# Optimization experiments

Measured on AMD Instinct MI355X. Metric: run time of the kernel, lower is better.

Reference implementation:

```python
import jax, jax.numpy as jnp
import numpy as np

B, C, H, G = 4, 128, 8, 64
F = G * G  # 4096 faces on a GxG grid mesh surrogate
DH = C // H


def _build_rings():
    # BFS rings on a GxG 4-neighbor grid from face 0 (corner): ring r = {(i,j): i+j == r}
    rings_list = []
    for r in range(2 * G - 1):
        lo, hi = max(0, r - G + 1), min(r, G - 1)
        rings_list.append([i * G + (r - i) for i in range(lo, hi + 1)])
    n_rings = len(rings_list)
    max_ring = max(len(rr) for rr in rings_list)
    rings = np.full((n_rings, max_ring), -1, dtype=np.int64)
    sizes = np.zeros((n_rings,), dtype=np.int64)
    for r, rr in enumerate(rings_list):
        rings[r, :len(rr)] = rr
        sizes[r] = len(rr)
    return rings, sizes


def setup_inputs() -> dict:
    key = jax.random.key(0)
    ks = jax.random.split(key, 6)
    s = 1.0 / np.sqrt(C)
    x = jax.random.normal(ks[0], (B, C, F), dtype=jnp.float32)
    Wq0 = jax.random.normal(ks[1], (C, C), dtype=jnp.float32) * s
    Wk0 = jax.random.normal(ks[2], (C, C), dtype=jnp.float32) * s
    Wv0 = jax.random.normal(ks[3], (C, C), dtype=jnp.float32) * s
    Wq1 = jax.random.normal(ks[4], (C, C), dtype=jnp.float32) * s
    Wk1 = jax.random.normal(ks[5], (C, C), dtype=jnp.float32) * s
    rings, sizes = _build_rings()
    return {"x": x, "Wq0": Wq0, "Wk0": Wk0, "Wv0": Wv0, "Wq1": Wq1, "Wk1": Wk1,
            "rings": jnp.asarray(rings), "ring_sizes": jnp.asarray(sizes)}


def _attend(q_in, kv_in, Wq, Wk, Wv):
    # AnchorAttentionBlock, mode='resid': MHA(q=q_in, kv=kv_in) + q_in
    Bq, Cc, Nq = q_in.shape
    Nk = kv_in.shape[2]
    q = jnp.einsum('oc,bcn->bon', Wq, q_in).reshape(Bq, H, DH, Nq)
    k = jnp.einsum('oc,bcn->bon', Wk, kv_in).reshape(Bq, H, DH, Nk)
    v = jnp.einsum('oc,bcn->bon', Wv, kv_in).reshape(Bq, H, DH, Nk)
    a = jax.nn.softmax(jnp.einsum('bhdq,bhdk->bhqk', q, k) / np.float32(np.sqrt(DH)), axis=-1)
    o = jnp.einsum('bhqk,bhdk->bhdq', a, v).reshape(Bq, Cc, Nq)
    return o + q_in


def _cos_map(q_in, kv_in, Wq, Wk):
    # return_map=True, normalize=True -> per-head cosine similarity map in [-1, 1]
    Bq, _, Nq = q_in.shape
    Nk = kv_in.shape[2]
    q = jnp.einsum('oc,bcn->bon', Wq, q_in).reshape(Bq, H, DH, Nq)
    k = jnp.einsum('oc,bcn->bon', Wk, kv_in).reshape(Bq, H, DH, Nk)
    qn = q * jax.lax.rsqrt(jnp.sum(q * q, axis=2, keepdims=True) + 1e-8)
    kn = k * jax.lax.rsqrt(jnp.sum(k * k, axis=2, keepdims=True) + 1e-8)
    return jnp.einsum('bhdq,bhdk->bhqk', qn, kn)  # [B,H,Nq,Nk]


def reference(x, Wq0, Wk0, Wv0, Wq1, Wk1, rings, ring_sizes):
    rings_np = np.asarray(rings)
    sizes_np = np.asarray(ring_sizes)
    feats = x
    # Sequential BFS flood-fill: per ring, boundary faces attend over all faces.
    # Vectorized over the batch (all meshes share the grid topology + anchor).
    for r in range(rings_np.shape[0]):
        ring = rings_np[r, :int(sizes_np[r])]          # concrete face indices of this ring
        bf = feats[:, :, ring]                          # [B, C, Nb] boundary features
        bf = _attend(bf, feats, Wq0, Wk0, Wv0)          # kv = all faces (current state)
        feats = feats.at[:, :, ring].set(bf)
    anchor = int(rings_np[0, 0])
    anchor_x = feats[:, :, anchor:anchor + 1]           # [B, C, 1]
    q_x = _attend(x, anchor_x, Wq0, Wk0, Wv0)           # attention[:-1] pass on raw x
    m = _cos_map(q_x, anchor_x, Wq1, Wk1)               # [B, H, F, 1] in [-1, 1]
    final_scores = jnp.mean((m + 1.0) * 0.5, axis=1)    # [B, F, 1] in [0, 1]
    return feats, final_scores
```

## Files before the change

### kernel.cpp

```cpp
#include <hip/hip_runtime.h>
#include <hip/hip_bf16.h>

#define Bn 4
#define Cn 128
#define Fn 4096
#define NRINGS 127

typedef short bhalf4 __attribute__((ext_vector_type(4)));
typedef float f32x4  __attribute__((ext_vector_type(4)));

#define OFF_K   1048576
#define OFF_V   2097152
#define OFF_PM  3145728
#define OFF_PL  3211264
#define OFF_PO  3276800
#define OFF_VA  4325376
#define OFF_KN  4325888

__device__ __forceinline__ ushort f2bf(float f) {
    __hip_bfloat16 h = __float2bfloat16(f);
    return *reinterpret_cast<ushort*>(&h);
}

__global__ __launch_bounds__(512, 2) void initQKV(
    const float* __restrict__ x, const float* __restrict__ Wq0,
    const float* __restrict__ Wk0, const float* __restrict__ Wv0,
    ushort* __restrict__ Q0bf, ushort* __restrict__ Kbf, ushort* __restrict__ Vbf)
{
    __shared__ float xs[Cn * 64];
    const int wg = blockIdx.x, t = threadIdx.x;
    const int b = wg >> 6, n0 = (wg & 63) << 6;
    for (int idx = t; idx < Cn * 64; idx += 512) {
        int c = idx >> 6, j = idx & 63;
        xs[idx] = x[(((b << 7) + c) << 12) + n0 + j];
    }
    __syncthreads();
    const int o = t & 127, j0 = (t >> 7) << 4;
    float aq[16], ak[16], av[16];
#pragma unroll
    for (int k = 0; k < 16; ++k) { aq[k] = 0.f; ak[k] = 0.f; av[k] = 0.f; }
    for (int c = 0; c < Cn; ++c) {
        float wq = Wq0[(o << 7) + c];
        float wk = Wk0[(o << 7) + c];
        float wv = Wv0[(o << 7) + c];
        const float* xr = &xs[(c << 6) + j0];
#pragma unroll
        for (int k = 0; k < 16; ++k) {
            float xv = xr[k];
            aq[k] += wq * xv; ak[k] += wk * xv; av[k] += wv * xv;
        }
    }
    const int h = o >> 4, d = o & 15;
    const int bh = (b << 3) + h;
#pragma unroll
    for (int k = 0; k < 16; ++k) {
        int col = n0 + j0 + k;
        int qi = ((bh << 12) + col) * 16 + d;
        Q0bf[qi] = f2bf(aq[k]);
        Kbf[qi]  = f2bf(ak[k]);
    }
    uint vv[8];
#pragma unroll
    for (int k2 = 0; k2 < 8; ++k2)
        vv[k2] = (uint)f2bf(av[2*k2]) | ((uint)f2bf(av[2*k2+1]) << 16);
    uint4* dst = (uint4*)&Vbf[(((bh << 4) + d) << 12) + n0 + j0];
    dst[0] = make_uint4(vv[0], vv[1], vv[2], vv[3]);
    dst[1] = make_uint4(vv[4], vv[5], vv[6], vv[7]);
}

template<bool TAIL>
__global__ __launch_bounds__(512, 2) void fusedRing(
    const float* __restrict__ x, const float* __restrict__ Wk0,
    const float* __restrict__ Wv0, const int* __restrict__ rings,
    const int* __restrict__ rsz, const ushort* __restrict__ Q0bf,
    ushort* __restrict__ Kbf, ushort* __restrict__ Vbf,
    float* __restrict__ pm, float* __restrict__ pl, float* __restrict__ po,
    float* __restrict__ feats, int r)
{
    __shared__ ushort Kls[512 * 24];
    __shared__ ushort Vls[16 * 520];
    __shared__ ushort Qls[64 * 24];
    __shared__ float  outc[4 * 128];
    __shared__ int colsC[64], colsF[64];
    __shared__ int ownIdx[64];
    __shared__ int ownCnt;

    const int t = threadIdx.x, wgid = blockIdx.x;
    const int b = wgid >> 6, h = (wgid >> 3) & 7, sp = wgid & 7;
    const int bh = (b << 3) + h;
    const int n  = TAIL ? 0 : rsz[r];
    const int np = (r > 0) ? rsz[r - 1] : 0;
    const int keybase = sp << 9;

    if (t < 64) colsC[t] = (r > 0 && t < np) ? rings[(r-1)*64 + t] : -1;
    else if (t < 128) { int q = t - 64; colsF[q] = (!TAIL && q < n) ? rings[r*64 + q] : -1; }
    if (t == 0) ownCnt = 0;
    __syncthreads();

    if (!TAIL) {
        {
            const uint4* src = (const uint4*)(Kbf + ((bh << 12) + keybase + t) * 16);
            uint4 a0 = src[0], a1 = src[1];
            *(uint4*)&Kls[t*24]     = a0;
            *(uint4*)&Kls[t*24 + 8] = a1;
        }
        {
            int d = t >> 5, c32 = t & 31;
            const uint4* src = (const uint4*)(Vbf + (((bh << 4) + d) << 12) + keybase + (c32 << 4));
            uint4 a0 = src[0], a1 = src[1];
            *(uint4*)&Vls[d*520 + (c32 << 4)]     = a0;
            *(uint4*)&Vls[d*520 + (c32 << 4) + 8] = a1;
        }
        if (t < 128) {
            int q = t >> 1, half = t & 1;
            int cq = colsF[q];
            uint4 qv = make_uint4(0u, 0u, 0u, 0u);
            if (cq >= 0)
                qv = *(const uint4*)(Q0bf + ((bh << 12) + cq) * 16 + half * 8);
            *(uint4*)&Qls[q*24 + half*8] = qv;
        }
    }
    __syncthreads();

    if (r > 0) {
        const int bufp = (r - 1) & 1;
        if (t < np) {
            int cq = colsC[t];
            if (cq >= keybase && cq < keybase + 512) {
                int slot = atomicAdd(&ownCnt, 1);
                ownIdx[slot] = t;
            }
        }
        __syncthreads();
        const int cnt = ownCnt;
        for (int base = 0; base < cnt; base += 4) {
            {
                int slot = t >> 7, c = t & 127;
                int ow = base + slot;
                if (ow < cnt) {
                    int j = ownIdx[ow];
                    int col = colsC[j];
                    int hh = c >> 4, dd = c & 15;
                    int p0 = ((bufp << 5) + (b << 3) + hh) * 1024 + j;
                    float mstar = -1e30f;
#pragma unroll
                    for (int s2 = 0; s2 < 16; ++s2)
                        mstar = fmaxf(mstar, pm[p0 + (s2 << 6)]);
                    float lstar = 0.f, osum = 0.f;
#pragma unroll
                    for (int s2 = 0; s2 < 16; ++s2) {
                        int pi = p0 + (s2 << 6);
                        float e = __expf(pm[pi] - mstar);
                        lstar += pl[pi] * e;
                        osum  += po[(pi << 4) + dd] * e;
                    }
                    float outv = osum / lstar + x[(((b << 7) + c) << 12) + col];
                    outc[(slot << 7) + c] = outv;
                    if (h == 0) feats[(((b << 7) + c) << 12) + col] = outv;
                }
            }
            __syncthreads();
            if (!TAIL && t < 128) {
                int slot = t >> 5;
                int ow = base + slot;
                if (ow < cnt) {
                    int task = t & 31;
                    int isV = task >> 4, dd = task & 15;
                    int col = colsC[ownIdx[ow]];
                    const float* W = isV ? Wv0 : Wk0;
                    const float* oc = &outc[slot << 7];
                    int row = (h << 4) + dd;
                    float acc = 0.f;
                    for (int c2 = 0; c2 < Cn; ++c2)
                        acc += W[(row << 7) + c2] * oc[c2];
                    ushort bfv = f2bf(acc);
                    if (isV) {
                        Vbf[(((bh << 4) + dd) << 12) + col] = bfv;
                        Vls[dd*520 + (col - keybase)] = bfv;
                    } else {
                        Kbf[((bh << 12) + col) * 16 + dd] = bfv;
                        Kls[(col - keybase)*24 + dd] = bfv;
                    }
                }
            }
            __syncthreads();
        }
    }
    if (TAIL) return;

    const int w = t >> 6, lane = t & 63;
    const int qt = w & 3, kh = w >> 2;
    const int buf = r & 1;
    if (qt * 16 < n) {
        const int lm = lane & 15, lg = lane >> 4;
        bhalf4 qf = *(const bhalf4*)&Qls[(qt*16 + lm)*24 + (lg << 2)];
        const int key0 = kh << 8;
        f32x4 sc[16];
#pragma unroll
        for (int kt = 0; kt < 16; ++kt) {
            bhalf4 kf = *(const bhalf4*)&Kls[(key0 + (kt << 4) + lm)*24 + (lg << 2)];
            f32x4 z = {0.f, 0.f, 0.f, 0.f};
            sc[kt] = __builtin_amdgcn_mfma_f32_16x16x16bf16_1k(kf, qf, z, 0, 0, 0);
        }
        float m = -1e30f;
#pragma unroll
        for (int kt = 0; kt < 16; ++kt) {
            m = fmaxf(m, fmaxf(fmaxf(sc[kt][0], sc[kt][1]), fmaxf(sc[kt][2], sc[kt][3])));
        }
        m = fmaxf(m, __shfl_xor(m, 16));
        m = fmaxf(m, __shfl_xor(m, 32));
        float lsum = 0.f;
        bhalf4 pf[16];
#pragma unroll
        for (int kt = 0; kt < 16; ++kt) {
            float p0 = __expf((sc[kt][0] - m) * 0.25f);
            float p1 = __expf((sc[kt][1] - m) * 0.25f);
            float p2 = __expf((sc[kt][2] - m) * 0.25f);
            float p3 = __expf((sc[kt][3] - m) * 0.25f);
            lsum += (p0 + p1) + (p2 + p3);
            bhalf4 pv;
            pv[0] = (short)f2bf(p0); pv[1] = (short)f2bf(p1);
            pv[2] = (short)f2bf(p2); pv[3] = (short)f2bf(p3);
            pf[kt] = pv;
        }
        lsum += __shfl_xor(lsum, 16);
        lsum += __shfl_xor(lsum, 32);
        f32x4 oacc = {0.f, 0.f, 0.f, 0.f};
#pragma unroll
        for (int kt = 0; kt < 16; ++kt) {
            bhalf4 vf = *(const bhalf4*)&Vls[lm*520 + key0 + (kt << 4) + (lg << 2)];
            oacc = __builtin_amdgcn_mfma_f32_16x16x16bf16_1k(pf[kt], vf, oacc, 0, 0, 0);
        }
        const int pb = ((((buf << 5) + bh) << 4) | ((sp << 1) + kh)) * 64;
        if (lg == 0) {
            pm[pb + qt*16 + lm] = m * 0.25f;
            pl[pb + qt*16 + lm] = lsum;
        }
#pragma unroll
        for (int reg = 0; reg < 4; ++reg)
            po[(pb + qt*16 + (lg << 2) + reg) * 16 + lm] = oacc[reg];
    }
}

__global__ __launch_bounds__(128) void epi1(
    const float* __restrict__ feats, const float* __restrict__ Wv0,
    const float* __restrict__ Wk1, const int* __restrict__ rings,
    float* __restrict__ Va, float* __restrict__ Kn)
{
    int b = blockIdx.x;
    int i = threadIdx.x;
    int anchor = rings[0];
    __shared__ float la[128];
    __shared__ float kk2[128];
    la[i] = feats[((b * Cn + i) << 12) + anchor];
    __syncthreads();
    float va = 0.f, k1 = 0.f;
    for (int c = 0; c < 128; ++c) {
        va += Wv0[i * 128 + c] * la[c];
        k1 += Wk1[i * 128 + c] * la[c];
    }
    Va[b * 128 + i] = va;
    kk2[i] = k1 * k1;
    __syncthreads();
    float ss = 0.f;
    int hb = i & ~15;
    for (int d = 0; d < 16; ++d) ss += kk2[hb + d];
    Kn[b * 128 + i] = k1 * rsqrtf(ss + 1e-8f);
}

__global__ __launch_bounds__(256) void epi2(
    const float* __restrict__ x, const float* __restrict__ Wq1,
    const float* __restrict__ Va, const float* __restrict__ Kn,
    float* __restrict__ scores)
{
    __shared__ float Wt[128 * 132];
    __shared__ float lxT[128 * 36];
    const int bid = blockIdx.x, t = threadIdx.x;
    const int b = bid >> 7, col0 = (bid & 127) << 5;
    for (int idx = t; idx < 128 * 128; idx += 256) {
        int o = idx >> 7, c = idx & 127;
        Wt[c*132 + o] = Wq1[idx];
    }
    for (int idx = t; idx < 128 * 32; idx += 256) {
        int c = idx >> 5, col = idx & 31;
        lxT[c*36 + col] = x[(((b << 7) + c) << 12) + col0 + col] + Va[(b << 7) + c];
    }
    __syncthreads();
    const int og = t & 31, colg = t >> 5;
    const int o0 = og << 2, cl0 = colg << 2;
    float acc[4][4];
#pragma unroll
    for (int i = 0; i < 4; ++i)
#pragma unroll
        for (int j = 0; j < 4; ++j) acc[i][j] = 0.f;
    for (int c = 0; c < 128; ++c) {
        f32x4 wv = *(const f32x4*)&Wt[c*132 + o0];
        f32x4 xv = *(const f32x4*)&lxT[c*36 + cl0];
#pragma unroll
        for (int i = 0; i < 4; ++i)
#pragma unroll
            for (int j = 0; j < 4; ++j) acc[i][j] += wv[i] * xv[j];
    }
    float kn4[4];
#pragma unroll
    for (int i = 0; i < 4; ++i) kn4[i] = Kn[(b << 7) + o0 + i];
    float res[4];
#pragma unroll
    for (int j = 0; j < 4; ++j) {
        float ss = acc[0][j]*acc[0][j] + acc[1][j]*acc[1][j]
                 + acc[2][j]*acc[2][j] + acc[3][j]*acc[3][j];
        ss += __shfl_xor(ss, 1);
        ss += __shfl_xor(ss, 2);
        float rs = rsqrtf(ss + 1e-8f);
        float mp = (acc[0][j]*kn4[0] + acc[1][j]*kn4[1]
                  + acc[2][j]*kn4[2] + acc[3][j]*kn4[3]) * rs;
#pragma unroll
        for (int msk = 1; msk <= 16; msk <<= 1) mp += __shfl_xor(mp, msk);
        res[j] = 0.5f + mp * (1.0f / 16.0f);
    }
    if (og == 0) {
#pragma unroll
        for (int j = 0; j < 4; ++j)
            scores[(b << 12) + col0 + cl0 + j] = res[j];
    }
}

extern "C" void kernel_launch(void* const* d_in, const int* in_sizes, int n_in,
                              void* d_out, int out_size, void* d_ws, size_t ws_size,
                              hipStream_t stream) {
    const float* x   = (const float*)d_in[0];
    const float* Wq0 = (const float*)d_in[1];
    const float* Wk0 = (const float*)d_in[2];
    const float* Wv0 = (const float*)d_in[3];
    const float* Wq1 = (const float*)d_in[4];
    const float* Wk1 = (const float*)d_in[5];
    const int*   rings = (const int*)d_in[6];
    const int*   rsz   = (const int*)d_in[7];

    float* feats  = (float*)d_out;
    float* scores = feats + Bn * Cn * Fn;

    float*  ws   = (float*)d_ws;
    ushort* Q0bf = (ushort*)ws;
    ushort* Kbf  = (ushort*)(ws + OFF_K);
    ushort* Vbf  = (ushort*)(ws + OFF_V);
    float*  pm   = ws + OFF_PM;
    float*  pl   = ws + OFF_PL;
    float*  po   = ws + OFF_PO;
    float*  Va   = ws + OFF_VA;
    float*  Kn   = ws + OFF_KN;

    initQKV<<<256, 512, 0, stream>>>(x, Wq0, Wk0, Wv0, Q0bf, Kbf, Vbf);

    for (int r = 0; r < NRINGS; ++r) {
        fusedRing<false><<<256, 512, 0, stream>>>(
            x, Wk0, Wv0, rings, rsz, Q0bf, Kbf, Vbf, pm, pl, po, feats, r);
    }
    fusedRing<true><<<256, 512, 0, stream>>>(
        x, Wk0, Wv0, rings, rsz, Q0bf, Kbf, Vbf, pm, pl, po, feats, NRINGS);

    epi1<<<Bn, 128, 0, stream>>>(feats, Wv0, Wk1, rings, Va, Kn);
    epi2<<<512, 256, 0, stream>>>(x, Wq1, Va, Kn, scores);
}
```

Baseline: 1.781 ms.

## Read K/V/Q fragments directly from global memory and parallelize ring K/V update

The ring kernel no longer stages the whole 512-key K and V slice and the Q tile into LDS on every launch. The MFMA loops now load fragments straight from global (L2-resident) buffers, and a threadfence plus barrier makes freshly written K/V visible first. The per-face K/V projection update is spread over all 512 threads, each summing a quarter of the channels with shuffle reductions. initQKV also tiles the weight matrices through LDS instead of reading them from global per thread. This trades a per-launch LDS fill and the extra barriers for scattered, less-coalesced global fragment loads.

```diff
diff --git a/kernel.cpp b/kernel.cpp
--- a/kernel.cpp
+++ b/kernel.cpp
@@ -28,28 +28,40 @@
     ushort* __restrict__ Q0bf, ushort* __restrict__ Kbf, ushort* __restrict__ Vbf)
 {
     __shared__ float xs[Cn * 64];
+    __shared__ float Wls[3 * 128 * 33];
     const int wg = blockIdx.x, t = threadIdx.x;
     const int b = wg >> 6, n0 = (wg & 63) << 6;
     for (int idx = t; idx < Cn * 64; idx += 512) {
         int c = idx >> 6, j = idx & 63;
         xs[idx] = x[(((b << 7) + c) << 12) + n0 + j];
     }
-    __syncthreads();
     const int o = t & 127, j0 = (t >> 7) << 4;
     float aq[16], ak[16], av[16];
 #pragma unroll
     for (int k = 0; k < 16; ++k) { aq[k] = 0.f; ak[k] = 0.f; av[k] = 0.f; }
-    for (int c = 0; c < Cn; ++c) {
-        float wq = Wq0[(o << 7) + c];
-        float wk = Wk0[(o << 7) + c];
-        float wv = Wv0[(o << 7) + c];
-        const float* xr = &xs[(c << 6) + j0];
-#pragma unroll
-        for (int k = 0; k < 16; ++k) {
-            float xv = xr[k];
-            aq[k] += wq * xv; ak[k] += wk * xv; av[k] += wv * xv;
-        }
-    }
+
+    for (int cc = 0; cc < 128; cc += 32) {
+        __syncthreads();
+        for (int idx = t; idx < 128 * 32; idx += 512) {
+            int oo = idx >> 5, jj = idx & 31;
+            Wls[oo * 33 + jj]                = Wq0[(oo << 7) + cc + jj];
+            Wls[128 * 33 + oo * 33 + jj]     = Wk0[(oo << 7) + cc + jj];
+            Wls[2 * 128 * 33 + oo * 33 + jj] = Wv0[(oo << 7) + cc + jj];
+        }
+        __syncthreads();
+        for (int c2 = 0; c2 < 32; ++c2) {
+            float wq = Wls[o * 33 + c2];
+            float wk = Wls[128 * 33 + o * 33 + c2];
+            float wv = Wls[2 * 128 * 33 + o * 33 + c2];
+            const float* xr = &xs[((cc + c2) << 6) + j0];
+#pragma unroll
+            for (int k = 0; k < 16; ++k) {
+                float xv = xr[k];
+                aq[k] += wq * xv; ak[k] += wk * xv; av[k] += wv * xv;
+            }
+        }
+    }
+
     const int h = o >> 4, d = o & 15;
     const int bh = (b << 3) + h;
 #pragma unroll
@@ -77,10 +89,7 @@
     float* __restrict__ pm, float* __restrict__ pl, float* __restrict__ po,
     float* __restrict__ feats, int r)
 {
-    __shared__ ushort Kls[512 * 24];
-    __shared__ ushort Vls[16 * 520];
-    __shared__ ushort Qls[64 * 24];
-    __shared__ float  outc[4 * 128];
+    __shared__ float outc[4 * 128];
     __shared__ int colsC[64], colsF[64];
     __shared__ int ownIdx[64];
     __shared__ int ownCnt;
@@ -93,33 +102,8 @@
     const int keybase = sp << 9;
 
     if (t < 64) colsC[t] = (r > 0 && t < np) ? rings[(r-1)*64 + t] : -1;
-    else if (t < 128) { int q = t - 64; colsF[q] = (!TAIL && q < n) ? rings[r*64 + q] : -1; }
+    else if (t < 128) { int q = t - 64; colsF[q] = (!TAIL && q < n) ? rings[r*64 + q] : 0; }
     if (t == 0) ownCnt = 0;
-    __syncthreads();
-
-    if (!TAIL) {
-        {
-            const uint4* src = (const uint4*)(Kbf + ((bh << 12) + keybase + t) * 16);
-            uint4 a0 = src[0], a1 = src[1];
-            *(uint4*)&Kls[t*24]     = a0;
-            *(uint4*)&Kls[t*24 + 8] = a1;
-        }
-        {
-            int d = t >> 5, c32 = t & 31;
-            const uint4* src = (const uint4*)(Vbf + (((bh << 4) + d) << 12) + keybase + (c32 << 4));
-            uint4 a0 = src[0], a1 = src[1];
-            *(uint4*)&Vls[d*520 + (c32 << 4)]     = a0;
-            *(uint4*)&Vls[d*520 + (c32 << 4) + 8] = a1;
-        }
-        if (t < 128) {
-            int q = t >> 1, half = t & 1;
-            int cq = colsF[q];
-            uint4 qv = make_uint4(0u, 0u, 0u, 0u);
-            if (cq >= 0)
-                qv = *(const uint4*)(Q0bf + ((bh << 12) + cq) * 16 + half * 8);
-            *(uint4*)&Qls[q*24 + half*8] = qv;
-        }
-    }
     __syncthreads();
 
     if (r > 0) {
@@ -160,26 +144,27 @@
                 }
             }
             __syncthreads();
-            if (!TAIL && t < 128) {
-                int slot = t >> 5;
+            if (!TAIL) {
+                int slot = t >> 7, rem = t & 127;
+                int task = rem >> 2, quarter = rem & 3;
                 int ow = base + slot;
                 if (ow < cnt) {
-                    int task = t & 31;
                     int isV = task >> 4, dd = task & 15;
                     int col = colsC[ownIdx[ow]];
+                    int row = (h << 4) + dd;
                     const float* W = isV ? Wv0 : Wk0;
                     const float* oc = &outc[slot << 7];
-                    int row = (h << 4) + dd;
                     float acc = 0.f;
-                    for (int c2 = 0; c2 < Cn; ++c2)
-                        acc += W[(row << 7) + c2] * oc[c2];
-                    ushort bfv = f2bf(acc);
-                    if (isV) {
-                        Vbf[(((bh << 4) + dd) << 12) + col] = bfv;
-                        Vls[dd*520 + (col - keybase)] = bfv;
-                    } else {
-                        Kbf[((bh << 12) + col) * 16 + dd] = bfv;
-                        Kls[(col - keybase)*24 + dd] = bfv;
+                    int c0 = quarter << 5;
+#pragma unroll
+                    for (int c2 = 0; c2 < 32; ++c2)
+                        acc += W[(row << 7) + c0 + c2] * oc[c0 + c2];
+                    acc += __shfl_xor(acc, 1);
+                    acc += __shfl_xor(acc, 2);
+                    if (quarter == 0) {
+                        ushort bfv = f2bf(acc);
+                        if (isV) Vbf[(((bh << 4) + dd) << 12) + col] = bfv;
+                        else     Kbf[((bh << 12) + col) * 16 + dd] = bfv;
                     }
                 }
             }
@@ -187,26 +172,30 @@
         }
     }
     if (TAIL) return;
+
+    __threadfence();
+    __syncthreads();
 
     const int w = t >> 6, lane = t & 63;
     const int qt = w & 3, kh = w >> 2;
     const int buf = r & 1;
     if (qt * 16 < n) {
         const int lm = lane & 15, lg = lane >> 4;
-        bhalf4 qf = *(const bhalf4*)&Qls[(qt*16 + lm)*24 + (lg << 2)];
-        const int key0 = kh << 8;
+        const int cq = colsF[qt * 16 + lm];
+        bhalf4 qf = *(const bhalf4*)&Q0bf[(((bh << 12) + cq) << 4) + (lg << 2)];
+        const int key0 = keybase + (kh << 8);
         f32x4 sc[16];
 #pragma unroll
         for (int kt = 0; kt < 16; ++kt) {
-            bhalf4 kf = *(const bhalf4*)&Kls[(key0 + (kt << 4) + lm)*24 + (lg << 2)];
+            bhalf4 kf = *(const bhalf4*)
+                &Kbf[(((bh << 12) + key0 + (kt << 4) + lm) << 4) + (lg << 2)];
             f32x4 z = {0.f, 0.f, 0.f, 0.f};
             sc[kt] = __builtin_amdgcn_mfma_f32_16x16x16bf16_1k(kf, qf, z, 0, 0, 0);
         }
         float m = -1e30f;
 #pragma unroll
-        for (int kt = 0; kt < 16; ++kt) {
+        for (int kt = 0; kt < 16; ++kt)
             m = fmaxf(m, fmaxf(fmaxf(sc[kt][0], sc[kt][1]), fmaxf(sc[kt][2], sc[kt][3])));
-        }
         m = fmaxf(m, __shfl_xor(m, 16));
         m = fmaxf(m, __shfl_xor(m, 32));
         float lsum = 0.f;
@@ -228,7 +217,8 @@
         f32x4 oacc = {0.f, 0.f, 0.f, 0.f};
 #pragma unroll
         for (int kt = 0; kt < 16; ++kt) {
-            bhalf4 vf = *(const bhalf4*)&Vls[lm*520 + key0 + (kt << 4) + (lg << 2)];
+            bhalf4 vf = *(const bhalf4*)
+                &Vbf[(((bh << 4) + lm) << 12) + key0 + (kt << 4) + (lg << 2)];
             oacc = __builtin_amdgcn_mfma_f32_16x16x16bf16_1k(pf[kt], vf, oacc, 0, 0, 0);
         }
         const int pb = ((((buf << 5) + bh) << 4) | ((sp << 1) + kh)) * 64;
```

Result: slower. 5.727 ms (+221.5%).

## Replace per-ring kernel launches with persistent cooperative kernel using grid barriers

Applied to the files above, without the earlier changes.

Runs the 127-ring sequential flood-fill inside one cooperative persistent kernel of 64 workgroups. Each workgroup keeps its 2048-key K/V slice resident in LDS across rings, and rings are separated by software global barriers instead of kernel launches. This is meant to remove per-launch overhead and the repeated reload of K/V tiles each ring. The cost is far fewer workgroups (64 vs 256), so each does more serial flash work, and it adds two spin barriers per ring. initQKV also now stages the weights through LDS in chunks, and the multi-launch path is kept as a fallback if the cooperative launch fails.

```diff
diff --git a/kernel.cpp b/kernel.cpp
--- a/kernel.cpp
+++ b/kernel.cpp
@@ -5,17 +5,20 @@
 #define Cn 128
 #define Fn 4096
 #define NRINGS 127
+#define NWG 64
 
 typedef short bhalf4 __attribute__((ext_vector_type(4)));
 typedef float f32x4  __attribute__((ext_vector_type(4)));
 
-#define OFF_K   1048576
-#define OFF_V   2097152
-#define OFF_PM  3145728
-#define OFF_PL  3211264
-#define OFF_PO  3276800
-#define OFF_VA  4325376
-#define OFF_KN  4325888
+#define OFF_K    1048576
+#define OFF_V    2097152
+#define OFF_PM   3145728
+#define OFF_PL   3211264
+#define OFF_PO   3276800
+#define OFF_OUTC 4325376
+#define OFF_VA   4358144
+#define OFF_KN   4358656
+#define OFF_BAR  4359168
 
 __device__ __forceinline__ ushort f2bf(float f) {
     __hip_bfloat16 h = __float2bfloat16(f);
@@ -25,29 +28,41 @@
 __global__ __launch_bounds__(512, 2) void initQKV(
     const float* __restrict__ x, const float* __restrict__ Wq0,
     const float* __restrict__ Wk0, const float* __restrict__ Wv0,
-    ushort* __restrict__ Q0bf, ushort* __restrict__ Kbf, ushort* __restrict__ Vbf)
+    ushort* __restrict__ Q0bf, ushort* __restrict__ Kbf, ushort* __restrict__ Vbf,
+    int* __restrict__ bar)
 {
     __shared__ float xs[Cn * 64];
+    __shared__ float Wls[3 * 128 * 33];
     const int wg = blockIdx.x, t = threadIdx.x;
+    if (wg == 0 && t == 0) bar[0] = 0;
     const int b = wg >> 6, n0 = (wg & 63) << 6;
     for (int idx = t; idx < Cn * 64; idx += 512) {
         int c = idx >> 6, j = idx & 63;
         xs[idx] = x[(((b << 7) + c) << 12) + n0 + j];
     }
-    __syncthreads();
     const int o = t & 127, j0 = (t >> 7) << 4;
     float aq[16], ak[16], av[16];
 #pragma unroll
     for (int k = 0; k < 16; ++k) { aq[k] = 0.f; ak[k] = 0.f; av[k] = 0.f; }
-    for (int c = 0; c < Cn; ++c) {
-        float wq = Wq0[(o << 7) + c];
-        float wk = Wk0[(o << 7) + c];
-        float wv = Wv0[(o << 7) + c];
-        const float* xr = &xs[(c << 6) + j0];
-#pragma unroll
-        for (int k = 0; k < 16; ++k) {
-            float xv = xr[k];
-            aq[k] += wq * xv; ak[k] += wk * xv; av[k] += wv * xv;
+    for (int cc = 0; cc < 128; cc += 32) {
+        __syncthreads();
+        for (int idx = t; idx < 128 * 32; idx += 512) {
+            int oo = idx >> 5, jj = idx & 31;
+            Wls[oo * 33 + jj]                = Wq0[(oo << 7) + cc + jj];
+            Wls[128 * 33 + oo * 33 + jj]     = Wk0[(oo << 7) + cc + jj];
+            Wls[2 * 128 * 33 + oo * 33 + jj] = Wv0[(oo << 7) + cc + jj];
+        }
+        __syncthreads();
+        for (int c2 = 0; c2 < 32; ++c2) {
+            float wq = Wls[o * 33 + c2];
+            float wk = Wls[128 * 33 + o * 33 + c2];
+            float wv = Wls[2 * 128 * 33 + o * 33 + c2];
+            const float* xr = &xs[((cc + c2) << 6) + j0];
+#pragma unroll
+            for (int k = 0; k < 16; ++k) {
+                float xv = xr[k];
+                aq[k] += wq * xv; ak[k] += wk * xv; av[k] += wv * xv;
+            }
         }
     }
     const int h = o >> 4, d = o & 15;
@@ -68,8 +83,223 @@
     dst[1] = make_uint4(vv[4], vv[5], vv[6], vv[7]);
 }
 
+__device__ __forceinline__ void gbar(int* bar, int target) {
+    __syncthreads();
+    if (threadIdx.x == 0) {
+        __threadfence();
+        __hip_atomic_fetch_add(bar, 1, __ATOMIC_RELEASE, __HIP_MEMORY_SCOPE_AGENT);
+        while (__hip_atomic_load(bar, __ATOMIC_RELAXED, __HIP_MEMORY_SCOPE_AGENT) < target)
+            __builtin_amdgcn_s_sleep(2);
+        __threadfence();
+    }
+    __syncthreads();
+}
+
+__device__ __forceinline__ void flashStep(
+    int n, int buf, int bh, int kv, int t,
+    const ushort* qs, const ushort* Kls, const ushort* Vls,
+    float* __restrict__ pm, float* __restrict__ pl, float* __restrict__ po)
+{
+    const int w = t >> 6, lane = t & 63;
+    const int qt = w & 3, kq = w >> 2;
+    if (qt * 16 >= n) return;
+    const int lm = lane & 15, lg = lane >> 4;
+    bhalf4 qf = *(const bhalf4*)&qs[(qt * 16 + lm) * 20 + (lg << 2)];
+    const int kbase = kq << 10;
+
+    float m = -3e38f;
+#pragma unroll 4
+    for (int kt = 0; kt < 64; ++kt) {
+        bhalf4 kf = *(const bhalf4*)&Kls[(kbase + (kt << 4) + lm) * 20 + (lg << 2)];
+        f32x4 z = {0.f, 0.f, 0.f, 0.f};
+        f32x4 s = __builtin_amdgcn_mfma_f32_16x16x16bf16_1k(kf, qf, z, 0, 0, 0);
+        m = fmaxf(m, fmaxf(fmaxf(s[0], s[1]), fmaxf(s[2], s[3])));
+    }
+    m = fmaxf(m, __shfl_xor(m, 16));
+    m = fmaxf(m, __shfl_xor(m, 32));
+
+    float lsum = 0.f;
+    f32x4 oacc = {0.f, 0.f, 0.f, 0.f};
+#pragma unroll 4
+    for (int kt = 0; kt < 64; ++kt) {
+        bhalf4 kf = *(const bhalf4*)&Kls[(kbase + (kt << 4) + lm) * 20 + (lg << 2)];
+        f32x4 z = {0.f, 0.f, 0.f, 0.f};
+        f32x4 s = __builtin_amdgcn_mfma_f32_16x16x16bf16_1k(kf, qf, z, 0, 0, 0);
+        float p0 = __expf((s[0] - m) * 0.25f);
+        float p1 = __expf((s[1] - m) * 0.25f);
+        float p2 = __expf((s[2] - m) * 0.25f);
+        float p3 = __expf((s[3] - m) * 0.25f);
+        lsum += (p0 + p1) + (p2 + p3);
+        bhalf4 pv;
+        pv[0] = (short)f2bf(p0); pv[1] = (short)f2bf(p1);
+        pv[2] = (short)f2bf(p2); pv[3] = (short)f2bf(p3);
+        bhalf4 vf = *(const bhalf4*)&Vls[lm * 2056 + kbase + (kt << 4) + (lg << 2)];
+        oacc = __builtin_amdgcn_mfma_f32_16x16x16bf16_1k(pv, vf, oacc, 0, 0, 0);
+    }
+    lsum += __shfl_xor(lsum, 16);
+    lsum += __shfl_xor(lsum, 32);
+
+    const int sl = (kv << 1) + kq;
+    const int pb = ((((buf << 5) + bh) << 2) + sl) * 64;
+    if (lg == 0) {
+        pm[pb + qt * 16 + lm] = m * 0.25f;
+        pl[pb + qt * 16 + lm] = lsum;
+    }
+#pragma unroll
+    for (int reg = 0; reg < 4; ++reg)
+        po[(pb + qt * 16 + (lg << 2) + reg) * 16 + lm] = oacc[reg];
+}
+
+__device__ __forceinline__ void combineP1(
+    int np, int bufp, int b, int h, int kv, int t,
+    const int* colsC, const float* __restrict__ x,
+    const float* __restrict__ pm, const float* __restrict__ pl,
+    const float* __restrict__ po, float* __restrict__ outcG,
+    float* __restrict__ feats)
+{
+    int jj = t >> 4, dd = t & 15;
+    int jq = (kv << 5) + jj;
+    if (jq >= np) return;
+    int bh = (b << 3) + h;
+    int col = colsC[jq];
+    int p0 = ((((bufp << 5) + bh) << 2) << 6) + jq;
+    float mstar = -3e38f;
+#pragma unroll
+    for (int sl = 0; sl < 4; ++sl) mstar = fmaxf(mstar, pm[p0 + (sl << 6)]);
+    float lstar = 0.f, osum = 0.f;
+#pragma unroll
+    for (int sl = 0; sl < 4; ++sl) {
+        int pi = p0 + (sl << 6);
+        float e = __expf(pm[pi] - mstar);
+        lstar += pl[pi] * e;
+        osum  += po[(pi << 4) + dd] * e;
+    }
+    float outv = osum / lstar + x[(((b << 7) + (h << 4) + dd) << 12) + col];
+    outcG[(((b << 6) + jq) << 7) + (h << 4) + dd] = outv;
+    feats[(((b << 7) + (h << 4) + dd) << 12) + col] = outv;
+}
+
+__device__ __forceinline__ void patchP2(
+    int np, int b, int h, int kv, int t,
+    const int* colsC, int* ownIdx, int* ownCnt,
+    const float* __restrict__ Wk0, const float* __restrict__ Wv0,
+    const float* __restrict__ outcG, ushort* Kls, ushort* Vls)
+{
+    const int keyG0 = kv << 11;
+    if (t < np) {
+        int cq = colsC[t];
+        if (cq >= keyG0 && cq < keyG0 + 2048)
+            ownIdx[atomicAdd(ownCnt, 1)] = t;
+    }
+    __syncthreads();
+    const int cnt = *ownCnt;
+    const int slot = t >> 6, rr = (t >> 1) & 31, half = t & 1;
+    const int dd = rr & 15;
+    for (int base = 0; base < cnt; base += 8) {
+        int ow = base + slot;
+        if (ow < cnt) {
+            int jq = ownIdx[ow];
+            int col = colsC[jq];
+            const float* W = (rr < 16) ? Wk0 : Wv0;
+            int row = (h << 4) + dd;
+            const f32x4* W4  = (const f32x4*)&W[(row << 7) + (half << 6)];
+            const f32x4* oc4 = (const f32x4*)&outcG[(((b << 6) + jq) << 7) + (half << 6)];
+            float acc = 0.f;
+#pragma unroll
+            for (int c4 = 0; c4 < 16; ++c4) {
+                f32x4 wv = W4[c4], xv = oc4[c4];
+                acc += wv[0]*xv[0] + wv[1]*xv[1] + wv[2]*xv[2] + wv[3]*xv[3];
+            }
+            acc += __shfl_xor(acc, 1);
+            if (half == 0) {
+                ushort bfv = f2bf(acc);
+                int colL = col - keyG0;
+                if (rr < 16) Kls[colL * 20 + dd] = bfv;
+                else         Vls[dd * 2056 + colL] = bfv;
+            }
+        }
+    }
+}
+
+__global__ __launch_bounds__(512, 1) void ringPersist(
+    const float* __restrict__ x, const float* __restrict__ Wk0,
+    const float* __restrict__ Wv0, const int* __restrict__ rings,
+    const int* __restrict__ rsz, const ushort* __restrict__ Q0bf,
+    const ushort* __restrict__ Kbf, const ushort* __restrict__ Vbf,
+    float* __restrict__ pm, float* __restrict__ pl, float* __restrict__ po,
+    float* __restrict__ outcG, float* __restrict__ feats, int* bar)
+{
+    __shared__ ushort Kls[2048 * 20];
+    __shared__ ushort Vls[16 * 2056];
+    __shared__ ushort qs[64 * 20];
+    __shared__ int colsC[64], colsF[64], ownIdx[64];
+    __shared__ int ownCnt;
+
+    const int wg = blockIdx.x, t = threadIdx.x;
+    const int b = wg >> 4, h = (wg >> 1) & 7, kv = wg & 1;
+    const int bh = (b << 3) + h;
+    const int keyG0 = kv << 11;
+    int bstep = 0;
+
+    for (int idx = t; idx < 2048 * 4; idx += 512) {
+        int key = idx >> 2, qtr = idx & 3;
+        *(uint2*)&Kls[key * 20 + (qtr << 2)] =
+            *(const uint2*)&Kbf[(((bh << 12) + keyG0 + key) << 4) + (qtr << 2)];
+    }
+    for (int idx = t; idx < 16 * 256; idx += 512) {
+        int d = idx >> 8, c8 = idx & 255;
+        *(uint4*)&Vls[d * 2056 + (c8 << 3)] =
+            *(const uint4*)&Vbf[(((bh << 4) + d) << 12) + keyG0 + (c8 << 3)];
+    }
+
+    {
+        const int n0r = rsz[0];
+        if (t < 64) colsF[t] = (t < n0r) ? rings[t] : 0;
+        __syncthreads();
+        if (t < 256) {
+            int j = t >> 2, qtr = t & 3;
+            int cq = colsF[j];
+            *(uint2*)&qs[j * 20 + (qtr << 2)] =
+                *(const uint2*)&Q0bf[(((bh << 12) + cq) << 4) + (qtr << 2)];
+        }
+        __syncthreads();
+        flashStep(n0r, 0, bh, kv, t, qs, Kls, Vls, pm, pl, po);
+    }
+
+    for (int r = 1; r < NRINGS; ++r) {
+        const int np = rsz[r - 1], n = rsz[r];
+        const int bufp = (r - 1) & 1;
+        gbar(bar, NWG * (++bstep));
+        if (t < 64) colsC[t] = (t < np) ? rings[(r - 1) * 64 + t] : -1;
+        else if (t < 128) colsF[t - 64] = (t - 64 < n) ? rings[r * 64 + t - 64] : 0;
+        if (t == 0) ownCnt = 0;
+        __syncthreads();
+        combineP1(np, bufp, b, h, kv, t, colsC, x, pm, pl, po, outcG, feats);
+        gbar(bar, NWG * (++bstep));
+        patchP2(np, b, h, kv, t, colsC, ownIdx, &ownCnt, Wk0, Wv0, outcG, Kls, Vls);
+        __syncthreads();
+        if (t < 256) {
+            int j = t >> 2, qtr = t & 3;
+            int cq = colsF[j];
+            *(uint2*)&qs[j * 20 + (qtr << 2)] =
+                *(const uint2*)&Q0bf[(((bh << 12) + cq) << 4) + (qtr << 2)];
+        }
+        __syncthreads();
+        flashStep(n, r & 1, bh, kv, t, qs, Kls, Vls, pm, pl, po);
+    }
+
+    {
+        gbar(bar, NWG * (++bstep));
+        const int np = rsz[NRINGS - 1];
+        if (t < 64) colsC[t] = (t < np) ? rings[(NRINGS - 1) * 64 + t] : -1;
+        __syncthreads();
+        combineP1(np, (NRINGS - 1) & 1, b, h, kv, t, colsC, x, pm, pl, po,
+                  outcG, feats);
+    }
+}
+
 template<bool TAIL>
-__global__ __launch_bounds__(512, 2) void fusedRing(
+__global__ __launch_bounds__(512, 2) void fusedRingFB(
     const float* __restrict__ x, const float* __restrict__ Wk0,
     const float* __restrict__ Wv0, const int* __restrict__ rings,
     const int* __restrict__ rsz, const ushort* __restrict__ Q0bf,
@@ -93,7 +323,7 @@
     const int keybase = sp << 9;
 
     if (t < 64) colsC[t] = (r > 0 && t < np) ? rings[(r-1)*64 + t] : -1;
-    else if (t < 128) { int q = t - 64; colsF[q] = (!TAIL && q < n) ? rings[r*64 + q] : -1; }
+    else if (t < 128) { int q = t - 64; colsF[q] = (!TAIL && q < n) ? rings[r*64 + q] : 0; }
     if (t == 0) ownCnt = 0;
     __syncthreads();
 
@@ -114,9 +344,7 @@
         if (t < 128) {
             int q = t >> 1, half = t & 1;
             int cq = colsF[q];
-            uint4 qv = make_uint4(0u, 0u, 0u, 0u);
-            if (cq >= 0)
-                qv = *(const uint4*)(Q0bf + ((bh << 12) + cq) * 16 + half * 8);
+            uint4 qv = *(const uint4*)(Q0bf + ((bh << 12) + cq) * 16 + half * 8);
             *(uint4*)&Qls[q*24 + half*8] = qv;
         }
     }
@@ -204,9 +432,8 @@
         }
         float m = -1e30f;
 #pragma unroll
-        for (int kt = 0; kt < 16; ++kt) {
+        for (int kt = 0; kt < 16; ++kt)
             m = fmaxf(m, fmaxf(fmaxf(sc[kt][0], sc[kt][1]), fmaxf(sc[kt][2], sc[kt][3])));
-        }
         m = fmaxf(m, __shfl_xor(m, 16));
         m = fmaxf(m, __shfl_xor(m, 32));
         float lsum = 0.f;
@@ -340,24 +567,34 @@
     float* feats  = (float*)d_out;
     float* scores = feats + Bn * Cn * Fn;
 
-    float*  ws   = (float*)d_ws;
-    ushort* Q0bf = (ushort*)ws;
-    ushort* Kbf  = (ushort*)(ws + OFF_K);
-    ushort* Vbf  = (ushort*)(ws + OFF_V);
-    float*  pm   = ws + OFF_PM;
-    float*  pl   = ws + OFF_PL;
-    float*  po   = ws + OFF_PO;
-    float*  Va   = ws + OFF_VA;
-    float*  Kn   = ws + OFF_KN;
-
-    initQKV<<<256, 512, 0, stream>>>(x, Wq0, Wk0, Wv0, Q0bf, Kbf, Vbf);
-
-    for (int r = 0; r < NRINGS; ++r) {
-        fusedRing<false><<<256, 512, 0, stream>>>(
-            x, Wk0, Wv0, rings, rsz, Q0bf, Kbf, Vbf, pm, pl, po, feats, r);
-    }
-    fusedRing<true><<<256, 512, 0, stream>>>(
-        x, Wk0, Wv0, rings, rsz, Q0bf, Kbf, Vbf, pm, pl, po, feats, NRINGS);
+    float*  ws    = (float*)d_ws;
+    ushort* Q0bf  = (ushort*)ws;
+    ushort* Kbf   = (ushort*)(ws + OFF_K);
+    ushort* Vbf   = (ushort*)(ws + OFF_V);
+    float*  pm    = ws + OFF_PM;
+    float*  pl    = ws + OFF_PL;
+    float*  po    = ws + OFF_PO;
+    float*  outcG = ws + OFF_OUTC;
+    float*  Va    = ws + OFF_VA;
+    float*  Kn    = ws + OFF_KN;
+    int*    bar   = (int*)(ws + OFF_BAR);
+
+    initQKV<<<256, 512, 0, stream>>>(x, Wq0, Wk0, Wv0, Q0bf, Kbf, Vbf, bar);
+
+    void* args[] = { (void*)&x, (void*)&Wk0, (void*)&Wv0, (void*)&rings,
+                     (void*)&rsz, (void*)&Q0bf, (void*)&Kbf, (void*)&Vbf,
+                     (void*)&pm, (void*)&pl, (void*)&po, (void*)&outcG,
+                     (void*)&feats, (void*)&bar };
+    hipError_t le = hipLaunchCooperativeKernel((void*)ringPersist, dim3(NWG),
+                                               dim3(512), args, 0, stream);
+    if (le != hipSuccess) {
+        for (int r = 0; r < NRINGS; ++r) {
+            fusedRingFB<false><<<256, 512, 0, stream>>>(
+                x, Wk0, Wv0, rings, rsz, Q0bf, Kbf, Vbf, pm, pl, po, feats, r);
+        }
+        fusedRingFB<true><<<256, 512, 0, stream>>>(
+            x, Wk0, Wv0, rings, rsz, Q0bf, Kbf, Vbf, pm, pl, po, feats, NRINGS);
+    }
 
     epi1<<<Bn, 128, 0, stream>>>(feats, Wv0, Wk1, rings, Va, Kn);
     epi2<<<512, 256, 0, stream>>>(x, Wq1, Va, Kn, scores);
```

After: 4.817 ms. 170% more time.
